# Optimization experiments

Hardware: AMD Instinct MI355X
Metric: run time of the kernel (lower is better)

The kernel has to match this reference:

```python
import jax, jax.numpy as jnp
import numpy as np
import math

B, S, D, H = 4, 2048, 768, 12
HD = D // H  # 64


def setup_inputs() -> dict:
    key = jax.random.key(0)
    ks = jax.random.split(key, 9)
    s = 0.02
    return {
        "hidden_states": jax.random.normal(ks[0], (B, S, D), jnp.float32),
        "layout_q": jax.random.normal(ks[1], (B, S, D), jnp.float32),
        "layout_k": jax.random.normal(ks[2], (B, S, D), jnp.float32),
        "attention_mask": jnp.zeros((B, 1, 1, S), jnp.float32),
        "Wq": jax.random.normal(ks[3], (D, D), jnp.float32) * s,
        "bq": jnp.zeros((D,), jnp.float32),
        "Wk": jax.random.normal(ks[4], (D, D), jnp.float32) * s,
        "bk": jnp.zeros((D,), jnp.float32),
        "Wv": jax.random.normal(ks[5], (D, D), jnp.float32) * s,
        "bv": jnp.zeros((D,), jnp.float32),
    }


def _split_heads(x):
    # [B,S,D] -> [B,H,S,HD]
    return x.reshape(B, S, H, HD).transpose(0, 2, 1, 3)


def reference(hidden_states, layout_q, layout_k, attention_mask, Wq, bq, Wk, bk, Wv, bv):
    q = _split_heads(hidden_states @ Wq.T + bq)
    k = _split_heads(hidden_states @ Wk.T + bk)
    v = _split_heads(hidden_states @ Wv.T + bv)
    lq = _split_heads(layout_q)
    lk = _split_heads(layout_k)
    scale = 1.0 / math.sqrt(HD)
    # dual-stream scores: content + layout, both [B,H,S,S]
    scores = (jnp.einsum("bhqd,bhkd->bhqk", q, k)
              + jnp.einsum("bhqd,bhkd->bhqk", lq, lk)) * scale
    scores = scores + attention_mask
    probs = jax.nn.softmax(scores, axis=-1)
    ctx = jnp.einsum("bhqk,bhkd->bhqd", probs, v)
    return ctx.transpose(0, 2, 1, 3).reshape(B, S, D)
```

## Files before the change

### kernel.cpp

```cpp
#include <hip/hip_runtime.h>


typedef __attribute__((ext_vector_type(8))) short short8;
typedef __attribute__((ext_vector_type(4))) float floatx4;

#define LOG2E 1.4426950408889634f
#define QSCL 0.18033688011112042f

static constexpr int Sn = 2048, Dn = 768, Hn = 12, BHn = 48;

__device__ __forceinline__ unsigned short f2bf(float f) {
  unsigned u = __float_as_uint(f);
  u += 0x7FFFu + ((u >> 16) & 1u);
  return (unsigned short)(u >> 16);
}

typedef const __attribute__((address_space(1))) unsigned int* gas_t;
typedef __attribute__((address_space(3))) unsigned int* las_t;
__device__ __forceinline__ void async16(const void* g, void* l) {
  __builtin_amdgcn_global_load_lds((gas_t)g, (las_t)l, 16, 0, 0);
}

__global__ void cast_hs_kernel(const float* __restrict__ in, unsigned short* __restrict__ out, int n4) {
  int i = blockIdx.x * 256 + threadIdx.x;
  if (i >= n4) return;
  float4 v = ((const float4*)in)[i];
  ushort4 o = make_ushort4(f2bf(v.x), f2bf(v.y), f2bf(v.z), f2bf(v.w));
  ((ushort4*)out)[i] = o;
}

__global__ void cast_w_kernel(const float* __restrict__ w0, const float* __restrict__ w1,
                              const float* __restrict__ w2, unsigned short* __restrict__ out) {
  int i = blockIdx.x * 256 + threadIdx.x;
  const float* src = (blockIdx.y == 0) ? w0 : (blockIdx.y == 1) ? w1 : w2;
  float4 v = ((const float4*)src)[i];
  ushort4 o = make_ushort4(f2bf(v.x), f2bf(v.y), f2bf(v.z), f2bf(v.w));
  ((ushort4*)(out + (size_t)blockIdx.y * Dn * Dn))[i] = o;
}

__global__ void pack_layout_kernel(const float* __restrict__ lq, const float* __restrict__ lk,
                                   unsigned short* __restrict__ Qc, unsigned short* __restrict__ Kc) {
  int idx = blockIdx.x * 256 + threadIdx.x;
  const float* src = blockIdx.y ? lk : lq;
  unsigned short* dst = blockIdx.y ? Kc : Qc;
  const float sc = blockIdx.y ? 1.0f : QSCL;
  int d4 = idx & 15;
  int t = idx >> 4;
  int h = t % Hn;
  int bs = t / Hn;
  int b = bs >> 11, s = bs & (Sn - 1);
  float4 v = ((const float4*)src)[idx];
  ushort4 o = make_ushort4(f2bf(v.x * sc), f2bf(v.y * sc), f2bf(v.z * sc), f2bf(v.w * sc));
  size_t off = ((size_t)(b * Hn + h) * Sn + s) * 128 + 64 + d4 * 4;
  *(ushort4*)(dst + off) = o;
}

__global__ __launch_bounds__(256, 2)
void proj_kernel(const unsigned short* __restrict__ X,
                 const unsigned short* __restrict__ Wb,
                 const float* __restrict__ bq, const float* __restrict__ bk, const float* __restrict__ bv,
                 unsigned short* __restrict__ Qc, unsigned short* __restrict__ Kc,
                 unsigned short* __restrict__ Vt) {
  __shared__ __align__(16) unsigned short sMem[16384];
  unsigned short* const sA = sMem;
  unsigned short* const sB = sMem + 8192;

  const int z = blockIdx.z;
  const unsigned short* W = Wb + (size_t)z * Dn * Dn;
  const float* bias = (z == 0) ? bq : (z == 1) ? bk : bv;

  const int t = threadIdx.x;
  const int lane = t & 63, wave = t >> 6;
  const int wm = wave >> 1, wn = wave & 1;
  const int quad = lane >> 4, col15 = lane & 15;
  const int m0 = blockIdx.y * 128, n0 = blockIdx.x * 128;

  const int srow = lane >> 3, schunk = lane & 7;

  floatx4 acc[4][4];
#pragma unroll
  for (int i = 0; i < 4; i++)
#pragma unroll
    for (int j = 0; j < 4; j++) acc[i][j] = (floatx4){0.f, 0.f, 0.f, 0.f};

  for (int k0 = 0; k0 < Dn; k0 += 64) {
    __syncthreads();
#pragma unroll
    for (int c = 0; c < 4; c++) {
      int row = wave * 32 + c * 8 + srow;
      int g = schunk ^ (row & 7);
      async16(X + (size_t)(m0 + row) * Dn + k0 + g * 8, sA + (wave * 32 + c * 8) * 64);
      async16(W + (size_t)(n0 + row) * Dn + k0 + g * 8, sB + (wave * 32 + c * 8) * 64);
    }
    __syncthreads();
#pragma unroll
    for (int kk = 0; kk < 2; kk++) {
      short8 af[4], bf[4];
      const int slot = ((kk * 4 + quad) ^ (col15 & 7)) * 8;
#pragma unroll
      for (int i = 0; i < 4; i++)
        af[i] = *(const short8*)(sA + (wm * 64 + i * 16 + col15) * 64 + slot);
#pragma unroll
      for (int j = 0; j < 4; j++)
        bf[j] = *(const short8*)(sB + (wn * 64 + j * 16 + col15) * 64 + slot);
#pragma unroll
      for (int i = 0; i < 4; i++)
#pragma unroll
        for (int j = 0; j < 4; j++)
          acc[i][j] = __builtin_amdgcn_mfma_f32_16x16x32_bf16(af[i], bf[j], acc[i][j], 0, 0, 0);
    }
  }

  __syncthreads();
  const int b = m0 >> 11;
  const int s0g = m0 & (Sn - 1);
  const int h0 = n0 >> 6;

  if (z < 2) {
    const float scl = (z == 0) ? QSCL : 1.0f;
    unsigned short* dst0 = (z == 0) ? Qc : Kc;
#pragma unroll
    for (int j = 0; j < 4; j++) {
      int nl = wn * 64 + j * 16 + col15;
      float bias_n = bias[n0 + nl];
#pragma unroll
      for (int i = 0; i < 4; i++) {
        int mb = wm * 64 + i * 16 + quad * 4;
#pragma unroll
        for (int r = 0; r < 4; r++) {
          int m = mb + r;
          sMem[m * 128 + (nl ^ (((m >> 2) & 3) << 4))] = f2bf((acc[i][j][r] + bias_n) * scl);
        }
      }
    }
    __syncthreads();
#pragma unroll
    for (int cc = 0; cc < 8; cc++) {
      int idx = cc * 256 + t;
      int m = idx >> 4, piece = idx & 15;
      int h = h0 + (piece >> 3), d8 = piece & 7;
      short8 v = *(const short8*)(sMem + m * 128 + (piece ^ (((m >> 2) & 3) << 1)) * 8);
      *(short8*)(dst0 + ((size_t)(b * Hn + h) * Sn + s0g + m) * 128 + d8 * 8) = v;
    }
  } else {
#pragma unroll
    for (int j = 0; j < 4; j++) {
      int nl = wn * 64 + j * 16 + col15;
      float bias_n = bias[n0 + nl];
#pragma unroll
      for (int i = 0; i < 4; i++) {
        int mb = wm * 64 + i * 16 + quad * 4;
        ushort4 pk = make_ushort4(f2bf(acc[i][j][0] + bias_n), f2bf(acc[i][j][1] + bias_n),
                                  f2bf(acc[i][j][2] + bias_n), f2bf(acc[i][j][3] + bias_n));
        *(ushort4*)(sMem + nl * 128 + (mb ^ ((nl & 7) << 4))) = pk;
      }
    }
    __syncthreads();
#pragma unroll
    for (int cc = 0; cc < 8; cc++) {
      int idx = cc * 256 + t;
      int nl = idx >> 4, piece = idx & 15;
      int h = h0 + (nl >> 6), d = nl & 63;
      short8 v = *(const short8*)(sMem + nl * 128 + (piece ^ ((nl & 7) << 1)) * 8);
      *(short8*)(Vt + ((size_t)(b * Hn + h) * 64 + d) * Sn + s0g + piece * 8) = v;
    }
  }
}

__global__ __launch_bounds__(256, 3)
void attn_kernel(const unsigned short* __restrict__ Qc,
                 const unsigned short* __restrict__ Kc,
                 const unsigned short* __restrict__ Vt,
                 const float* __restrict__ mask,
                 float* __restrict__ out) {
  constexpr int LDV = 72;
  __shared__ __align__(16) unsigned short sKc[64 * 128];
  __shared__ __align__(16) unsigned short sVt[64 * 64];
  __shared__ __align__(16) unsigned short sS[128 * LDV];

  const int t = threadIdx.x;
  const int lane = t & 63, wave = t >> 6;
  const int quad = lane >> 4, col15 = lane & 15;

  const int id = blockIdx.x;
  const int slot = id >> 3;
  const int bh = (id & 7) + 8 * (slot >> 4);
  const int q0 = (slot & 15) * 128;
  const int b = bh / Hn, h = bh % Hn;

  short8 aq[2][4];
  const unsigned short* Qbase = Qc + ((size_t)bh * Sn + q0) * 128;
#pragma unroll
  for (int i = 0; i < 2; i++)
#pragma unroll
    for (int kk = 0; kk < 4; kk++)
      aq[i][kk] = *(const short8*)(Qbase + (size_t)(wave * 32 + i * 16 + col15) * 128 + kk * 32 + quad * 8);

  floatx4 O[2][4];
#pragma unroll
  for (int i = 0; i < 2; i++)
#pragma unroll
    for (int j = 0; j < 4; j++) O[i][j] = (floatx4){0.f, 0.f, 0.f, 0.f};
  float lsum[2][4];
#pragma unroll
  for (int i = 0; i < 2; i++)
#pragma unroll
    for (int r = 0; r < 4; r++) lsum[i][r] = 0.f;

  const unsigned short* Kbase = Kc + (size_t)bh * Sn * 128;
  const unsigned short* Vbase = Vt + (size_t)bh * 64 * Sn;
  const float* mbase = mask + (size_t)b * Sn;

  const int krow = lane >> 4, kslot = lane & 15;
  const int vrow = lane >> 3, vslot = lane & 7;

  for (int kt = 0; kt < Sn / 64; kt++) {
    __syncthreads();
#pragma unroll
    for (int c = 0; c < 4; c++) {
      int row = wave * 16 + c * 4 + krow;
      int g = (kslot & 8) | ((kslot ^ row) & 7);
      async16(Kbase + (size_t)(kt * 64 + row) * 128 + g * 8, sKc + (wave * 16 + c * 4) * 128);
    }
#pragma unroll
    for (int c = 0; c < 2; c++) {
      int row = wave * 16 + c * 8 + vrow;
      int g = vslot ^ (row & 7);
      async16(Vbase + (size_t)row * Sn + kt * 64 + g * 8, sVt + (wave * 16 + c * 8) * 64);
    }
    float mvalL[4];
#pragma unroll
    for (int jk = 0; jk < 4; jk++)
      mvalL[jk] = mbase[kt * 64 + jk * 16 + col15] * LOG2E;
    __syncthreads();

    floatx4 sacc[2][4];
#pragma unroll
    for (int jk = 0; jk < 4; jk++) {
      sacc[0][jk] = (floatx4){0.f, 0.f, 0.f, 0.f};
      sacc[1][jk] = (floatx4){0.f, 0.f, 0.f, 0.f};
#pragma unroll
      for (int kk = 0; kk < 4; kk++) {
        int slot_ = (((kk * 4 + quad) & 8) | (((kk * 4 + quad) ^ col15) & 7)) * 8;
        short8 bk_ = *(const short8*)(sKc + (jk * 16 + col15) * 128 + slot_);
        sacc[0][jk] = __builtin_amdgcn_mfma_f32_16x16x32_bf16(aq[0][kk], bk_, sacc[0][jk], 0, 0, 0);
        sacc[1][jk] = __builtin_amdgcn_mfma_f32_16x16x32_bf16(aq[1][kk], bk_, sacc[1][jk], 0, 0, 0);
      }
    }

#pragma unroll
    for (int i = 0; i < 2; i++) {
      int rowb = wave * 32 + i * 16 + quad * 4;
#pragma unroll
      for (int jk = 0; jk < 4; jk++) {
        int colb = jk * 16 + col15;
#pragma unroll
        for (int r = 0; r < 4; r++) {
          float p = __builtin_amdgcn_exp2f(sacc[i][jk][r] + mvalL[jk]);
          unsigned pu = __float_as_uint(p) & 0xFFFF0000u;
          lsum[i][r] += __uint_as_float(pu);
          sS[(rowb + r) * LDV + colb] = (unsigned short)(pu >> 16);
        }
      }
    }

#pragma unroll
    for (int kk = 0; kk < 2; kk++) {
      short8 ap0 = *(const short8*)(sS + (wave * 32 + col15) * LDV + kk * 32 + quad * 8);
      short8 ap1 = *(const short8*)(sS + (wave * 32 + 16 + col15) * LDV + kk * 32 + quad * 8);
      const int vslot_r = ((kk * 4 + quad) ^ (col15 & 7)) * 8;
#pragma unroll
      for (int j = 0; j < 4; j++) {
        short8 bv_ = *(const short8*)(sVt + (j * 16 + col15) * 64 + vslot_r);
        O[0][j] = __builtin_amdgcn_mfma_f32_16x16x32_bf16(ap0, bv_, O[0][j], 0, 0, 0);
        O[1][j] = __builtin_amdgcn_mfma_f32_16x16x32_bf16(ap1, bv_, O[1][j], 0, 0, 0);
      }
    }
  }

#pragma unroll
  for (int i = 0; i < 2; i++) {
#pragma unroll
    for (int r = 0; r < 4; r++) {
      float s_ = lsum[i][r];
      s_ += __shfl_xor(s_, 1);
      s_ += __shfl_xor(s_, 2);
      s_ += __shfl_xor(s_, 4);
      s_ += __shfl_xor(s_, 8);
      lsum[i][r] = 1.0f / s_;
    }
    int rowb = wave * 32 + i * 16 + quad * 4;
#pragma unroll
    for (int j = 0; j < 4; j++) {
      int dcol = h * 64 + j * 16 + col15;
      float* obase = out + ((size_t)b * Sn + q0 + rowb) * Dn + dcol;
      obase[0 * Dn] = O[i][j][0] * lsum[i][0];
      obase[1 * Dn] = O[i][j][1] * lsum[i][1];
      obase[2 * Dn] = O[i][j][2] * lsum[i][2];
      obase[3 * Dn] = O[i][j][3] * lsum[i][3];
    }
  }
}

extern "C" void kernel_launch(void* const* d_in, const int* in_sizes, int n_in,
                              void* d_out, int out_size, void* d_ws, size_t ws_size,
                              hipStream_t stream) {
  const float* hs   = (const float*)d_in[0];
  const float* lq   = (const float*)d_in[1];
  const float* lk   = (const float*)d_in[2];
  const float* mask = (const float*)d_in[3];
  const float* Wq   = (const float*)d_in[4];
  const float* bq   = (const float*)d_in[5];
  const float* Wk   = (const float*)d_in[6];
  const float* bk   = (const float*)d_in[7];
  const float* Wv   = (const float*)d_in[8];
  const float* bv   = (const float*)d_in[9];
  float* out = (float*)d_out;

  char* ws = (char*)d_ws;
  unsigned short* Xbf = (unsigned short*)ws;
  unsigned short* Wbf = (unsigned short*)(ws + 12582912);
  unsigned short* Qc  = (unsigned short*)(ws + 12582912 + 3538944);
  unsigned short* Kc  = Qc + (size_t)BHn * Sn * 128;
  unsigned short* Vt  = Kc + (size_t)BHn * Sn * 128;

  cast_hs_kernel<<<6144, 256, 0, stream>>>(hs, Xbf, 1572864);
  cast_w_kernel<<<dim3(576, 3), 256, 0, stream>>>(Wq, Wk, Wv, Wbf);
  pack_layout_kernel<<<dim3(6144, 2), 256, 0, stream>>>(lq, lk, Qc, Kc);
  proj_kernel<<<dim3(6, 64, 3), 256, 0, stream>>>(Xbf, Wbf, bq, bk, bv, Qc, Kc, Vt);
  attn_kernel<<<768, 256, 0, stream>>>(Qc, Kc, Vt, mask, out);
}
```

Measured before the change: 269.6 us.

## Retile attention to two waves with 64 query rows each and remap projection grid

The attention kernel now runs 128 threads per block: two waves each own 64 query rows, and keys are processed in 32-key tiles, so every K/V fragment loaded from LDS feeds four MFMA row tiles instead of two. The projection kernel switches to a 1D grid whose block index is decoded so that consecutive M-tiles land on the same XCD, aiming for better L2 locality on X, and its occupancy hint rises to 3 blocks. The larger per-wave accumulator state raises register pressure. Halving the key tile doubles the number of barrier and load iterations, and the P matrix is now read back with split 8-byte LDS loads.

```diff
diff --git a/kernel.cpp b/kernel.cpp
--- a/kernel.cpp
+++ b/kernel.cpp
@@ -55,7 +55,7 @@
   *(ushort4*)(dst + off) = o;
 }
 
-__global__ __launch_bounds__(256, 2)
+__global__ __launch_bounds__(256, 3)
 void proj_kernel(const unsigned short* __restrict__ X,
                  const unsigned short* __restrict__ Wb,
                  const float* __restrict__ bq, const float* __restrict__ bk, const float* __restrict__ bv,
@@ -65,7 +65,15 @@
   unsigned short* const sA = sMem;
   unsigned short* const sB = sMem + 8192;
 
-  const int z = blockIdx.z;
+  const unsigned id = blockIdx.x;
+  const unsigned xcd = id & 7;
+  const unsigned slot = id >> 3;
+  const unsigned yloc = slot / 18;
+  const unsigned rem = slot - yloc * 18;
+  const unsigned z = rem / 6;
+  const unsigned xb = rem - z * 6;
+  const int m0 = (int)(xcd * 8 + yloc) * 128, n0 = (int)xb * 128;
+
   const unsigned short* W = Wb + (size_t)z * Dn * Dn;
   const float* bias = (z == 0) ? bq : (z == 1) ? bk : bv;
 
@@ -73,7 +81,6 @@
   const int lane = t & 63, wave = t >> 6;
   const int wm = wave >> 1, wn = wave & 1;
   const int quad = lane >> 4, col15 = lane & 15;
-  const int m0 = blockIdx.y * 128, n0 = blockIdx.x * 128;
 
   const int srow = lane >> 3, schunk = lane & 7;
 
@@ -96,13 +103,13 @@
 #pragma unroll
     for (int kk = 0; kk < 2; kk++) {
       short8 af[4], bf[4];
-      const int slot = ((kk * 4 + quad) ^ (col15 & 7)) * 8;
+      const int slot_ = ((kk * 4 + quad) ^ (col15 & 7)) * 8;
 #pragma unroll
       for (int i = 0; i < 4; i++)
-        af[i] = *(const short8*)(sA + (wm * 64 + i * 16 + col15) * 64 + slot);
+        af[i] = *(const short8*)(sA + (wm * 64 + i * 16 + col15) * 64 + slot_);
 #pragma unroll
       for (int j = 0; j < 4; j++)
-        bf[j] = *(const short8*)(sB + (wn * 64 + j * 16 + col15) * 64 + slot);
+        bf[j] = *(const short8*)(sB + (wn * 64 + j * 16 + col15) * 64 + slot_);
 #pragma unroll
       for (int i = 0; i < 4; i++)
 #pragma unroll
@@ -167,15 +174,15 @@
   }
 }
 
-__global__ __launch_bounds__(256, 3)
+__global__ __launch_bounds__(128, 2)
 void attn_kernel(const unsigned short* __restrict__ Qc,
                  const unsigned short* __restrict__ Kc,
                  const unsigned short* __restrict__ Vt,
                  const float* __restrict__ mask,
                  float* __restrict__ out) {
-  constexpr int LDV = 72;
-  __shared__ __align__(16) unsigned short sKc[64 * 128];
-  __shared__ __align__(16) unsigned short sVt[64 * 64];
+  constexpr int LDV = 40;
+  __shared__ __align__(16) unsigned short sKc[32 * 128];
+  __shared__ __align__(16) unsigned short sVt[64 * 32];
   __shared__ __align__(16) unsigned short sS[128 * LDV];
 
   const int t = threadIdx.x;
@@ -188,22 +195,22 @@
   const int q0 = (slot & 15) * 128;
   const int b = bh / Hn, h = bh % Hn;
 
-  short8 aq[2][4];
-  const unsigned short* Qbase = Qc + ((size_t)bh * Sn + q0) * 128;
-#pragma unroll
-  for (int i = 0; i < 2; i++)
+  short8 aq[4][4];
+  const unsigned short* Qbase = Qc + ((size_t)bh * Sn + q0 + wave * 64) * 128;
+#pragma unroll
+  for (int i = 0; i < 4; i++)
 #pragma unroll
     for (int kk = 0; kk < 4; kk++)
-      aq[i][kk] = *(const short8*)(Qbase + (size_t)(wave * 32 + i * 16 + col15) * 128 + kk * 32 + quad * 8);
-
-  floatx4 O[2][4];
-#pragma unroll
-  for (int i = 0; i < 2; i++)
+      aq[i][kk] = *(const short8*)(Qbase + (size_t)(i * 16 + col15) * 128 + kk * 32 + quad * 8);
+
+  floatx4 O[4][4];
+#pragma unroll
+  for (int i = 0; i < 4; i++)
 #pragma unroll
     for (int j = 0; j < 4; j++) O[i][j] = (floatx4){0.f, 0.f, 0.f, 0.f};
-  float lsum[2][4];
-#pragma unroll
-  for (int i = 0; i < 2; i++)
+  float lsum[4][4];
+#pragma unroll
+  for (int i = 0; i < 4; i++)
 #pragma unroll
     for (int r = 0; r < 4; r++) lsum[i][r] = 0.f;
 
@@ -212,47 +219,51 @@
   const float* mbase = mask + (size_t)b * Sn;
 
   const int krow = lane >> 4, kslot = lane & 15;
-  const int vrow = lane >> 3, vslot = lane & 7;
-
-  for (int kt = 0; kt < Sn / 64; kt++) {
+  const int vrow = lane >> 2, vchunk = lane & 3;
+
+  for (int kt = 0; kt < Sn / 32; kt++) {
     __syncthreads();
 #pragma unroll
     for (int c = 0; c < 4; c++) {
       int row = wave * 16 + c * 4 + krow;
       int g = (kslot & 8) | ((kslot ^ row) & 7);
-      async16(Kbase + (size_t)(kt * 64 + row) * 128 + g * 8, sKc + (wave * 16 + c * 4) * 128);
+      async16(Kbase + (size_t)(kt * 32 + row) * 128 + g * 8, sKc + (wave * 16 + c * 4) * 128);
     }
 #pragma unroll
     for (int c = 0; c < 2; c++) {
-      int row = wave * 16 + c * 8 + vrow;
-      int g = vslot ^ (row & 7);
-      async16(Vbase + (size_t)row * Sn + kt * 64 + g * 8, sVt + (wave * 16 + c * 8) * 64);
-    }
-    float mvalL[4];
-#pragma unroll
-    for (int jk = 0; jk < 4; jk++)
-      mvalL[jk] = mbase[kt * 64 + jk * 16 + col15] * LOG2E;
-    __syncthreads();
-
-    floatx4 sacc[2][4];
-#pragma unroll
-    for (int jk = 0; jk < 4; jk++) {
-      sacc[0][jk] = (floatx4){0.f, 0.f, 0.f, 0.f};
-      sacc[1][jk] = (floatx4){0.f, 0.f, 0.f, 0.f};
+      int row = wave * 32 + c * 16 + vrow;
+      int g = vchunk ^ (row & 3);
+      async16(Vbase + (size_t)row * Sn + kt * 32 + g * 8, sVt + (wave * 32 + c * 16) * 32);
+    }
+    float mvalL[2];
+#pragma unroll
+    for (int jk = 0; jk < 2; jk++)
+      mvalL[jk] = mbase[kt * 32 + jk * 16 + col15] * LOG2E;
+    __syncthreads();
+
+    floatx4 sacc[4][2];
+#pragma unroll
+    for (int i = 0; i < 4; i++) {
+      sacc[i][0] = (floatx4){0.f, 0.f, 0.f, 0.f};
+      sacc[i][1] = (floatx4){0.f, 0.f, 0.f, 0.f};
+    }
+#pragma unroll
+    for (int jk = 0; jk < 2; jk++)
 #pragma unroll
       for (int kk = 0; kk < 4; kk++) {
-        int slot_ = (((kk * 4 + quad) & 8) | (((kk * 4 + quad) ^ col15) & 7)) * 8;
-        short8 bk_ = *(const short8*)(sKc + (jk * 16 + col15) * 128 + slot_);
-        sacc[0][jk] = __builtin_amdgcn_mfma_f32_16x16x32_bf16(aq[0][kk], bk_, sacc[0][jk], 0, 0, 0);
-        sacc[1][jk] = __builtin_amdgcn_mfma_f32_16x16x32_bf16(aq[1][kk], bk_, sacc[1][jk], 0, 0, 0);
-      }
-    }
-
-#pragma unroll
-    for (int i = 0; i < 2; i++) {
-      int rowb = wave * 32 + i * 16 + quad * 4;
-#pragma unroll
-      for (int jk = 0; jk < 4; jk++) {
+        int row = jk * 16 + col15;
+        int slot_ = (((kk * 4 + quad) & 8) | (((kk * 4 + quad) ^ row) & 7)) * 8;
+        short8 bk_ = *(const short8*)(sKc + row * 128 + slot_);
+#pragma unroll
+        for (int i = 0; i < 4; i++)
+          sacc[i][jk] = __builtin_amdgcn_mfma_f32_16x16x32_bf16(aq[i][kk], bk_, sacc[i][jk], 0, 0, 0);
+      }
+
+#pragma unroll
+    for (int i = 0; i < 4; i++) {
+      int rowb = wave * 64 + i * 16 + quad * 4;
+#pragma unroll
+      for (int jk = 0; jk < 2; jk++) {
         int colb = jk * 16 + col15;
 #pragma unroll
         for (int r = 0; r < 4; r++) {
@@ -265,21 +276,23 @@
     }
 
 #pragma unroll
-    for (int kk = 0; kk < 2; kk++) {
-      short8 ap0 = *(const short8*)(sS + (wave * 32 + col15) * LDV + kk * 32 + quad * 8);
-      short8 ap1 = *(const short8*)(sS + (wave * 32 + 16 + col15) * LDV + kk * 32 + quad * 8);
-      const int vslot_r = ((kk * 4 + quad) ^ (col15 & 7)) * 8;
+    for (int i = 0; i < 4; i++) {
+      const unsigned short* sp = sS + (wave * 64 + i * 16 + col15) * LDV + quad * 8;
+      ushort4 lo = *(const ushort4*)sp;
+      ushort4 hi = *(const ushort4*)(sp + 4);
+      short8 ap = {(short)lo.x, (short)lo.y, (short)lo.z, (short)lo.w,
+                   (short)hi.x, (short)hi.y, (short)hi.z, (short)hi.w};
 #pragma unroll
       for (int j = 0; j < 4; j++) {
-        short8 bv_ = *(const short8*)(sVt + (j * 16 + col15) * 64 + vslot_r);
-        O[0][j] = __builtin_amdgcn_mfma_f32_16x16x32_bf16(ap0, bv_, O[0][j], 0, 0, 0);
-        O[1][j] = __builtin_amdgcn_mfma_f32_16x16x32_bf16(ap1, bv_, O[1][j], 0, 0, 0);
+        int row = j * 16 + col15;
+        short8 bv_ = *(const short8*)(sVt + row * 32 + (quad ^ (row & 3)) * 8);
+        O[i][j] = __builtin_amdgcn_mfma_f32_16x16x32_bf16(ap, bv_, O[i][j], 0, 0, 0);
       }
     }
   }
 
 #pragma unroll
-  for (int i = 0; i < 2; i++) {
+  for (int i = 0; i < 4; i++) {
 #pragma unroll
     for (int r = 0; r < 4; r++) {
       float s_ = lsum[i][r];
@@ -289,7 +302,7 @@
       s_ += __shfl_xor(s_, 8);
       lsum[i][r] = 1.0f / s_;
     }
-    int rowb = wave * 32 + i * 16 + quad * 4;
+    int rowb = wave * 64 + i * 16 + quad * 4;
 #pragma unroll
     for (int j = 0; j < 4; j++) {
       int dcol = h * 64 + j * 16 + col15;
@@ -327,6 +340,6 @@
   cast_hs_kernel<<<6144, 256, 0, stream>>>(hs, Xbf, 1572864);
   cast_w_kernel<<<dim3(576, 3), 256, 0, stream>>>(Wq, Wk, Wv, Wbf);
   pack_layout_kernel<<<dim3(6144, 2), 256, 0, stream>>>(lq, lk, Qc, Kc);
-  proj_kernel<<<dim3(6, 64, 3), 256, 0, stream>>>(Xbf, Wbf, bq, bk, bv, Qc, Kc, Vt);
-  attn_kernel<<<768, 256, 0, stream>>>(Qc, Kc, Vt, mask, out);
-}
+  proj_kernel<<<1152, 256, 0, stream>>>(Xbf, Wbf, bq, bk, bv, Qc, Kc, Vt);
+  attn_kernel<<<768, 128, 0, stream>>>(Qc, Kc, Vt, mask, out);
+}
```

Result: slower. 293.7 us (+9.0%).

## Compute transposed scores to keep probabilities in registers, drop LDS P round-trip

Applied to the files above, without the earlier changes.

The attention kernel now computes S^T (K as the A operand, Q as B), so each lane's exp'd probabilities already match the B-operand layout of a 16x16x16 bf16 MFMA. P·V becomes V^T·P^T and runs from registers, which removes the shared-memory P staging buffer, its stores and reloads, and the extra syncs. The mask row is also preloaded into LDS once per block instead of being read from global on every tile. The output is stored as float4 vectors. The trade-off is twice as many MFMA issues, because the K=16 instruction replaces the K=32 one for PV.

```diff
diff --git a/kernel.cpp b/kernel.cpp
--- a/kernel.cpp
+++ b/kernel.cpp
@@ -2,6 +2,7 @@
 
 
 typedef __attribute__((ext_vector_type(8))) short short8;
+typedef __attribute__((ext_vector_type(4))) short short4v;
 typedef __attribute__((ext_vector_type(4))) float floatx4;
 
 #define LOG2E 1.4426950408889634f
@@ -19,6 +20,15 @@
 typedef __attribute__((address_space(3))) unsigned int* las_t;
 __device__ __forceinline__ void async16(const void* g, void* l) {
   __builtin_amdgcn_global_load_lds((gas_t)g, (las_t)l, 16, 0, 0);
+}
+
+__device__ __forceinline__ floatx4 mfma16(short4v a, short4v b, floatx4 c) {
+#if __has_builtin(__builtin_amdgcn_mfma_f32_16x16x16bf16_1k)
+  return __builtin_amdgcn_mfma_f32_16x16x16bf16_1k(a, b, c, 0, 0, 0);
+#else
+  asm volatile("v_mfma_f32_16x16x16_bf16 %0, %1, %2, %0" : "+v"(c) : "v"(a), "v"(b));
+  return c;
+#endif
 }
 
 __global__ void cast_hs_kernel(const float* __restrict__ in, unsigned short* __restrict__ out, int n4) {
@@ -96,13 +106,13 @@
 #pragma unroll
     for (int kk = 0; kk < 2; kk++) {
       short8 af[4], bf[4];
-      const int slot = ((kk * 4 + quad) ^ (col15 & 7)) * 8;
+      const int slot_ = ((kk * 4 + quad) ^ (col15 & 7)) * 8;
 #pragma unroll
       for (int i = 0; i < 4; i++)
-        af[i] = *(const short8*)(sA + (wm * 64 + i * 16 + col15) * 64 + slot);
+        af[i] = *(const short8*)(sA + (wm * 64 + i * 16 + col15) * 64 + slot_);
 #pragma unroll
       for (int j = 0; j < 4; j++)
-        bf[j] = *(const short8*)(sB + (wn * 64 + j * 16 + col15) * 64 + slot);
+        bf[j] = *(const short8*)(sB + (wn * 64 + j * 16 + col15) * 64 + slot_);
 #pragma unroll
       for (int i = 0; i < 4; i++)
 #pragma unroll
@@ -173,10 +183,9 @@
                  const unsigned short* __restrict__ Vt,
                  const float* __restrict__ mask,
                  float* __restrict__ out) {
-  constexpr int LDV = 72;
   __shared__ __align__(16) unsigned short sKc[64 * 128];
   __shared__ __align__(16) unsigned short sVt[64 * 64];
-  __shared__ __align__(16) unsigned short sS[128 * LDV];
+  __shared__ __align__(16) float sMask[Sn];
 
   const int t = threadIdx.x;
   const int lane = t & 63, wave = t >> 6;
@@ -188,28 +197,29 @@
   const int q0 = (slot & 15) * 128;
   const int b = bh / Hn, h = bh % Hn;
 
+  const float* mbase = mask + (size_t)b * Sn;
+#pragma unroll
+  for (int c = 0; c < 2; c++)
+    async16(mbase + (c * 256 + wave * 64 + lane) * 4, sMask + (c * 256 + wave * 64) * 4);
+
   short8 aq[2][4];
-  const unsigned short* Qbase = Qc + ((size_t)bh * Sn + q0) * 128;
-#pragma unroll
-  for (int i = 0; i < 2; i++)
+  const unsigned short* Qbase = Qc + ((size_t)bh * Sn + q0 + wave * 32) * 128;
+#pragma unroll
+  for (int jq = 0; jq < 2; jq++)
 #pragma unroll
     for (int kk = 0; kk < 4; kk++)
-      aq[i][kk] = *(const short8*)(Qbase + (size_t)(wave * 32 + i * 16 + col15) * 128 + kk * 32 + quad * 8);
-
-  floatx4 O[2][4];
-#pragma unroll
-  for (int i = 0; i < 2; i++)
-#pragma unroll
-    for (int j = 0; j < 4; j++) O[i][j] = (floatx4){0.f, 0.f, 0.f, 0.f};
-  float lsum[2][4];
-#pragma unroll
-  for (int i = 0; i < 2; i++)
-#pragma unroll
-    for (int r = 0; r < 4; r++) lsum[i][r] = 0.f;
+      aq[jq][kk] = *(const short8*)(Qbase + (size_t)(jq * 16 + col15) * 128 + kk * 32 + quad * 8);
+
+  floatx4 OT[4][2];
+#pragma unroll
+  for (int i = 0; i < 4; i++) {
+    OT[i][0] = (floatx4){0.f, 0.f, 0.f, 0.f};
+    OT[i][1] = (floatx4){0.f, 0.f, 0.f, 0.f};
+  }
+  float lsum[2] = {0.f, 0.f};
 
   const unsigned short* Kbase = Kc + (size_t)bh * Sn * 128;
   const unsigned short* Vbase = Vt + (size_t)bh * 64 * Sn;
-  const float* mbase = mask + (size_t)b * Sn;
 
   const int krow = lane >> 4, kslot = lane & 15;
   const int vrow = lane >> 3, vslot = lane & 7;
@@ -228,76 +238,75 @@
       int g = vslot ^ (row & 7);
       async16(Vbase + (size_t)row * Sn + kt * 64 + g * 8, sVt + (wave * 16 + c * 8) * 64);
     }
-    float mvalL[4];
-#pragma unroll
-    for (int jk = 0; jk < 4; jk++)
-      mvalL[jk] = mbase[kt * 64 + jk * 16 + col15] * LOG2E;
-    __syncthreads();
-
-    floatx4 sacc[2][4];
+    __syncthreads();
+
+    floatx4 sacc[4][2];
 #pragma unroll
     for (int jk = 0; jk < 4; jk++) {
-      sacc[0][jk] = (floatx4){0.f, 0.f, 0.f, 0.f};
-      sacc[1][jk] = (floatx4){0.f, 0.f, 0.f, 0.f};
+      sacc[jk][0] = (floatx4){0.f, 0.f, 0.f, 0.f};
+      sacc[jk][1] = (floatx4){0.f, 0.f, 0.f, 0.f};
 #pragma unroll
       for (int kk = 0; kk < 4; kk++) {
-        int slot_ = (((kk * 4 + quad) & 8) | (((kk * 4 + quad) ^ col15) & 7)) * 8;
-        short8 bk_ = *(const short8*)(sKc + (jk * 16 + col15) * 128 + slot_);
-        sacc[0][jk] = __builtin_amdgcn_mfma_f32_16x16x32_bf16(aq[0][kk], bk_, sacc[0][jk], 0, 0, 0);
-        sacc[1][jk] = __builtin_amdgcn_mfma_f32_16x16x32_bf16(aq[1][kk], bk_, sacc[1][jk], 0, 0, 0);
-      }
-    }
-
-#pragma unroll
-    for (int i = 0; i < 2; i++) {
-      int rowb = wave * 32 + i * 16 + quad * 4;
+        int gr = kk * 4 + quad;
+        int slot_ = ((gr & 8) | ((gr ^ col15) & 7)) * 8;
+        short8 kf = *(const short8*)(sKc + (jk * 16 + col15) * 128 + slot_);
+        sacc[jk][0] = __builtin_amdgcn_mfma_f32_16x16x32_bf16(kf, aq[0][kk], sacc[jk][0], 0, 0, 0);
+        sacc[jk][1] = __builtin_amdgcn_mfma_f32_16x16x32_bf16(kf, aq[1][kk], sacc[jk][1], 0, 0, 0);
+      }
+    }
+
+    short4v pvb[2][4];
+#pragma unroll
+    for (int jk = 0; jk < 4; jk++) {
+      float4 mv = *(const float4*)(sMask + kt * 64 + jk * 16 + quad * 4);
+      float m0 = mv.x * LOG2E, m1 = mv.y * LOG2E, m2 = mv.z * LOG2E, m3 = mv.w * LOG2E;
+#pragma unroll
+      for (int jq = 0; jq < 2; jq++) {
+        unsigned u0 = __float_as_uint(__builtin_amdgcn_exp2f(sacc[jk][jq][0] + m0)) & 0xFFFF0000u;
+        unsigned u1 = __float_as_uint(__builtin_amdgcn_exp2f(sacc[jk][jq][1] + m1)) & 0xFFFF0000u;
+        unsigned u2 = __float_as_uint(__builtin_amdgcn_exp2f(sacc[jk][jq][2] + m2)) & 0xFFFF0000u;
+        unsigned u3 = __float_as_uint(__builtin_amdgcn_exp2f(sacc[jk][jq][3] + m3)) & 0xFFFF0000u;
+        lsum[jq] += (__uint_as_float(u0) + __uint_as_float(u1)) +
+                    (__uint_as_float(u2) + __uint_as_float(u3));
+        int2 pk;
+        pk.x = (int)((u0 >> 16) | u1);
+        pk.y = (int)((u2 >> 16) | u3);
+        pvb[jq][jk] = *(short4v*)&pk;
+      }
+    }
+
+#pragma unroll
+    for (int i = 0; i < 4; i++) {
+      int row = i * 16 + col15;
 #pragma unroll
       for (int jk = 0; jk < 4; jk++) {
-        int colb = jk * 16 + col15;
-#pragma unroll
-        for (int r = 0; r < 4; r++) {
-          float p = __builtin_amdgcn_exp2f(sacc[i][jk][r] + mvalL[jk]);
-          unsigned pu = __float_as_uint(p) & 0xFFFF0000u;
-          lsum[i][r] += __uint_as_float(pu);
-          sS[(rowb + r) * LDV + colb] = (unsigned short)(pu >> 16);
-        }
-      }
-    }
-
-#pragma unroll
-    for (int kk = 0; kk < 2; kk++) {
-      short8 ap0 = *(const short8*)(sS + (wave * 32 + col15) * LDV + kk * 32 + quad * 8);
-      short8 ap1 = *(const short8*)(sS + (wave * 32 + 16 + col15) * LDV + kk * 32 + quad * 8);
-      const int vslot_r = ((kk * 4 + quad) ^ (col15 & 7)) * 8;
-#pragma unroll
-      for (int j = 0; j < 4; j++) {
-        short8 bv_ = *(const short8*)(sVt + (j * 16 + col15) * 64 + vslot_r);
-        O[0][j] = __builtin_amdgcn_mfma_f32_16x16x32_bf16(ap0, bv_, O[0][j], 0, 0, 0);
-        O[1][j] = __builtin_amdgcn_mfma_f32_16x16x32_bf16(ap1, bv_, O[1][j], 0, 0, 0);
-      }
-    }
-  }
-
-#pragma unroll
-  for (int i = 0; i < 2; i++) {
-#pragma unroll
-    for (int r = 0; r < 4; r++) {
-      float s_ = lsum[i][r];
-      s_ += __shfl_xor(s_, 1);
-      s_ += __shfl_xor(s_, 2);
-      s_ += __shfl_xor(s_, 4);
-      s_ += __shfl_xor(s_, 8);
-      lsum[i][r] = 1.0f / s_;
-    }
-    int rowb = wave * 32 + i * 16 + quad * 4;
-#pragma unroll
-    for (int j = 0; j < 4; j++) {
-      int dcol = h * 64 + j * 16 + col15;
-      float* obase = out + ((size_t)b * Sn + q0 + rowb) * Dn + dcol;
-      obase[0 * Dn] = O[i][j][0] * lsum[i][0];
-      obase[1 * Dn] = O[i][j][1] * lsum[i][1];
-      obase[2 * Dn] = O[i][j][2] * lsum[i][2];
-      obase[3 * Dn] = O[i][j][3] * lsum[i][3];
+        int gi = (jk * 2 + (quad >> 1)) ^ (row & 7);
+        short4v vf = *(const short4v*)(sVt + row * 64 + gi * 8 + (quad & 1) * 4);
+        OT[i][0] = mfma16(vf, pvb[0][jk], OT[i][0]);
+        OT[i][1] = mfma16(vf, pvb[1][jk], OT[i][1]);
+      }
+    }
+  }
+
+  float linv[2];
+#pragma unroll
+  for (int jq = 0; jq < 2; jq++) {
+    float s_ = lsum[jq];
+    s_ += __shfl_xor(s_, 16);
+    s_ += __shfl_xor(s_, 32);
+    linv[jq] = 1.0f / s_;
+  }
+#pragma unroll
+  for (int jq = 0; jq < 2; jq++) {
+    float* obase = out + ((size_t)b * Sn + q0 + wave * 32 + jq * 16 + col15) * Dn + h * 64 + quad * 4;
+#pragma unroll
+    for (int i = 0; i < 4; i++) {
+      float4 o;
+      o.x = OT[i][jq][0] * linv[jq];
+      o.y = OT[i][jq][1] * linv[jq];
+      o.z = OT[i][jq][2] * linv[jq];
+      o.w = OT[i][jq][3] * linv[jq];
+      *(float4*)(obase + i * 16) = o;
     }
   }
 }
```

Measured after the change: 272.9 us. About the same (+1.3%).
